# Kernel optimization log

Measured on AMD Instinct MI355X. Metric: run time of the kernel, lower is better.

## Reference

```python
import jax, jax.numpy as jnp
import numpy as np

E, L, M, F, S, P = 4, 10, 512, 128, 1000, 10  # envs, labels, max_sample, features, sample_size, batch_len


def setup_inputs() -> dict:
    key = jax.random.key(0)
    k1, k2, k3 = jax.random.split(key, 3)
    data_len = jax.random.randint(k1, (E, L), M // 2, M + 1, dtype=jnp.int32)
    matrix = jax.random.normal(k2, (E, L, M, F), dtype=jnp.float32)
    # zero out padded samples beyond data_len (as shape_to_matrix does)
    pad_mask = jnp.arange(M)[None, None, :, None] < data_len[:, :, None, None]
    matrix = matrix * pad_mask
    params = jnp.eye(F, dtype=jnp.float32) + 0.01 * jax.random.normal(k3, (F, F), dtype=jnp.float32)
    is_train_env = jnp.array([True, True, False, False])
    return {"matrix": matrix, "params": params, "data_len": data_len, "is_train_env": is_train_env}


def reference(matrix, params, data_len, is_train_env):
    lenf = data_len.astype(matrix.dtype)  # [E,L], torch keeps this as float32
    # __init__ preprocessing: normalize by mean std over sample dim (detached in torch)
    std = jax.lax.stop_gradient(jnp.std(matrix, axis=2).mean())
    mat = matrix / std
    # Silverman-style bandwidth on the normalized matrix (detached in torch)
    bw = jax.lax.stop_gradient(1.06 * (M ** (-1.0 / 5.0)) * jnp.std(mat, axis=2).mean())
    offset = jnp.exp(-0.5 / bw ** 2)
    proj = jnp.einsum('elmf,fg->elmg', mat, params)  # [E,L,M,F]
    left = jax.lax.stop_gradient(proj.min())   # .item() in torch -> constant
    right = jax.lax.stop_gradient(proj.max())
    delta = (right - left) / S
    x_grid = jnp.linspace(left, right, S)
    divisor = jnp.sqrt(2.0 * jnp.pi) * bw

    def step(acc, points):  # points: [P] grid chunk
        d2 = (proj[..., None] - points) ** 2                     # [E,L,M,F,P]
        s = jnp.sum(offset ** d2, axis=2)                        # [E,L,F,P]
        # remove contribution of zero-padded samples, then normalize by true count
        corr = (M - lenf)[:, :, None] * (offset ** (points ** 2))[None, None, :]  # [E,L,P]
        r = (s - corr[:, :, None, :]) / lenf[:, :, None, None]   # [E,L,F,P]
        d = jnp.sum(jnp.abs(r[:, None] - r[None, :]), axis=-1)   # [E,E,L,F] pairwise L1 over grid chunk
        return acc + d, None

    store_dis, _ = jax.lax.scan(step, jnp.zeros((E, E, L, F), proj.dtype), x_grid.reshape(S // P, P))
    store_dis = store_dis / divisor  # [E,E,L,F]

    idx = jnp.arange(E)
    upper = idx[:, None] < idx[None, :]                                   # all env pairs i<j
    train_pair = upper & is_train_env[:, None] & is_train_env[None, :]    # train env pairs i<j
    half = store_dis * (delta / 2.0)
    neg = jnp.array(-jnp.inf, half.dtype)
    test_results = jnp.where(upper[:, :, None, None], half, neg).max(axis=(0, 1))        # [L,F]
    train_results = jnp.where(train_pair[:, :, None, None], half, neg).max(axis=(0, 1))  # [L,F]
    train_dis = train_results.max(axis=0).mean()
    test_dis = test_results.max(axis=0).mean()
    return train_results, test_results, train_dis, test_dis
```

## Files before the change

kernel.cpp:

```cpp
#include <hip/hip_runtime.h>
#include <cmath>

#define E_ 4
#define L_ 10
#define M_ 512
#define F_ 128
#define S_ 1000

typedef unsigned int u32;
typedef _Float16 f16;
typedef __attribute__((ext_vector_type(8))) _Float16 v8h;
typedef __attribute__((ext_vector_type(4))) float v4f;

__device__ __forceinline__ float fexp2(float a){
#if __has_builtin(__builtin_amdgcn_exp2f)
  return __builtin_amdgcn_exp2f(a);
#else
  return exp2f(a);
#endif
}


__global__ __launch_bounds__(256) void k_pre(const float* __restrict__ mat,
                       const float* __restrict__ par,
                       float* __restrict__ projT, float* __restrict__ wsf){
  __shared__ float sm[512];
  int b = blockIdx.x, tid = threadIdx.x;
  if (b >= 1280){
    int el = b - 1280;
    int f = tid & 127, part = tid >> 7;
    const float* base = mat + ((size_t)el * M_ + part*256) * F_;
    float s = 0.f, s2 = 0.f;
    for (int i = 0; i < 256; i++){
      float v = base[i*F_ + f];
      s += v; s2 += v*v;
    }
    sm[tid] = s; sm[256 + tid] = s2;
    __syncthreads();
    if (tid < 128){
      wsf[2576 + el*128 + tid] = sm[tid] + sm[tid+128];
      wsf[7696 + el*128 + tid] = sm[256+tid] + sm[256+tid+128];
    }
    return;
  }
  int el = b >> 5, mt = (b & 31) * 16;
  int lane = tid & 63, wave = tid >> 6;
  int q = (lane >> 4) & 3, m16 = lane & 15;
  const float* arow = mat + ((size_t)el * M_ + mt + m16) * F_;
  v4f acc0 = {0.f,0.f,0.f,0.f}, acc1 = {0.f,0.f,0.f,0.f};
  #pragma unroll
  for (int c = 0; c < 4; c++){
    float4 a0 = *(const float4*)&arow[c*32 + q*8];
    float4 a1 = *(const float4*)&arow[c*32 + q*8 + 4];
    v8h af, b0, b1;
    af[0]=(f16)a0.x; af[1]=(f16)a0.y; af[2]=(f16)a0.z; af[3]=(f16)a0.w;
    af[4]=(f16)a1.x; af[5]=(f16)a1.y; af[6]=(f16)a1.z; af[7]=(f16)a1.w;
    const float* pb = par + (c*32 + q*8)*F_ + wave*32 + m16;
    #pragma unroll
    for (int j = 0; j < 8; j++){
      b0[j] = (f16)pb[j*F_];
      b1[j] = (f16)pb[j*F_ + 16];
    }
    acc0 = __builtin_amdgcn_mfma_f32_16x16x32_f16(af, b0, acc0, 0, 0, 0);
    acc1 = __builtin_amdgcn_mfma_f32_16x16x32_f16(af, b1, acc1, 0, 0, 0);
  }
  *(float4*)(projT + ((size_t)el*F_ + wave*32      + m16)*M_ + mt + q*4)
      = make_float4(acc0[0], acc0[1], acc0[2], acc0[3]);
  *(float4*)(projT + ((size_t)el*F_ + wave*32 + 16 + m16)*M_ + mt + q*4)
      = make_float4(acc1[0], acc1[1], acc1[2], acc1[3]);
  float lmin =  3.4e38f, lmax = -3.4e38f;
  #pragma unroll
  for (int r = 0; r < 4; r++){
    lmin = fminf(lmin, fminf(acc0[r], acc1[r]));
    lmax = fmaxf(lmax, fmaxf(acc0[r], acc1[r]));
  }
  #pragma unroll
  for (int d = 32; d >= 1; d >>= 1){
    lmin = fminf(lmin, __shfl_xor(lmin, d, 64));
    lmax = fmaxf(lmax, __shfl_xor(lmax, d, 64));
  }
  if (lane == 0){ sm[wave] = lmin; sm[8+wave] = lmax; }
  __syncthreads();
  if (tid == 0){
    wsf[16   + b] = fminf(fminf(sm[0], sm[1]), fminf(sm[2], sm[3]));
    wsf[1296 + b] = fmaxf(fmaxf(sm[8], sm[9]), fmaxf(sm[10], sm[11]));
  }
}

__global__ __launch_bounds__(1024) void k_red(float* __restrict__ wsf, float divisor){
  __shared__ float rmn[1024], rmx[1024], rs[1024];
  int tid = threadIdx.x;
  float mn = 3.4e38f, mx = -3.4e38f, s = 0.f;
  for (int i = tid; i < 1280; i += 1024){
    mn = fminf(mn, wsf[16   + i]);
    mx = fmaxf(mx, wsf[1296 + i]);
  }
  for (int i = tid; i < 5120; i += 1024){
    float a  = wsf[2576 + i];
    float a2 = wsf[7696 + i];
    float mean = a * (1.0f/512.0f);
    float var  = a2 * (1.0f/512.0f) - mean*mean;
    s += sqrtf(fmaxf(var, 0.0f));
  }
  rmn[tid] = mn; rmx[tid] = mx; rs[tid] = s;
  __syncthreads();
  for (int g = 512; g >= 1; g >>= 1){
    if (tid < g){
      rmn[tid] = fminf(rmn[tid], rmn[tid+g]);
      rmx[tid] = fmaxf(rmx[tid], rmx[tid+g]);
      rs[tid] += rs[tid+g];
    }
    __syncthreads();
  }
  if (tid == 0){
    float rstd   = 5120.0f / rs[0];
    float leftS  = rmn[0] * rstd;
    float rightS = rmx[0] * rstd;
    float stepFS = (rightS - leftS) * (1.0f/999.0f);
    float inv2   = 1.0f / (2.0f * stepFS);
    wsf[0] = rstd * inv2;
    wsf[1] = leftS * inv2;
    wsf[2] = stepFS;
    wsf[3] = leftS;
    wsf[8] = ((rightS - leftS) * (1.0f/1000.0f)) * 0.5f / divisor;
  }
}

__global__ __launch_bounds__(256) void k_kde(const float* __restrict__ projT,
                      const int* __restrict__ dlen, const float* __restrict__ wsf,
                      float* __restrict__ dpair, float k2c){
  __shared__ __align__(16) float smem[5104];
  int b = blockIdx.x;
  int l = b >> 7, f = b & 127;
  int tid = threadIdx.x, wave = tid >> 6, lane = tid & 63;
  for (int idx = tid; idx < 512; idx += 256){
    int e = idx >> 7, mq = idx & 127;
    ((float4*)smem)[idx] =
      ((const float4*)(projT + (((size_t)e * L_ + l) * F_ + f) * M_))[mq];
  }
  float posScale = wsf[0], posOff = wsf[1], stepFS = wsf[2], leftS = wsf[3];
  for (int idx = tid; idx < 656; idx += 256)
    ((float4*)(smem + 2048))[idx] = make_float4(0.f,0.f,0.f,0.f);
  float sh = 2.0f * stepFS;
  if (tid < 72){
    int u = tid - 34;
    float d0 = (float)(2*u)   * sh;
    float d1 = (float)(2*u-1) * sh;
    float2 t = (tid < 69) ? make_float2(fexp2(k2c*d0*d0), fexp2(k2c*d1*d1))
                          : make_float2(0.f, 0.f);
    *(float2*)&smem[4672 + 2*tid] = t;
  }
  {
    float xc = fmaf((float)(tid - 1), 4.0f*stepFS, leftS);
    smem[4816 + tid] = fexp2(k2c * xc * xc);
  }
  __syncthreads();
  {
    float* hf = smem + 2048 + wave*656;
    const float4* spw4 = (const float4*)(smem + wave*512);
    float4 p0 = spw4[lane], p1 = spw4[lane + 64];
    float pv[8] = {p0.x,p0.y,p0.z,p0.w,p1.x,p1.y,p1.z,p1.w};
    #pragma unroll
    for (int i = 0; i < 8; i++){
      float pos = fmaf(pv[i], posScale, -posOff);
      float n = floorf(pos + 0.5f);
      float d = pos - n;
      float wm = 0.5f*(0.5f-d)*(0.5f-d);
      float wp = 0.5f*(0.5f+d)*(0.5f+d);
      float w0 = 0.75f - d*d;
      int base = (int)n + 71;
      atomicAdd(&hf[base  ], wm);
      atomicAdd(&hf[base+1], w0);
      atomicAdd(&hf[base+2], wp);
    }
  }
  __syncthreads();
  float lenE = (float)dlen[wave*L_ + l];
  float rlen = 1.0f / lenE;
  float padc = 512.0f - lenE;
  {
    const float* sK = smem + 4672;
    const float* hb = smem + 2048 + wave*656;
    float a0=0.f, a1=0.f, a2=0.f, a3=0.f;
    #pragma unroll 8
    for (int uu = 0; uu < 72; uu++){
      float2 kv = *(const float2*)&sK[2*uu];
      int off = 2*(69 - uu) + 2*lane;
      float2 h0 = *(const float2*)&hb[off];
      float2 h1 = *(const float2*)&hb[off + 128];
      float2 h2 = *(const float2*)&hb[off + 256];
      float2 h3 = *(const float2*)&hb[off + 384];
      a0 = fmaf(h0.x, kv.x, fmaf(h0.y, kv.y, a0));
      a1 = fmaf(h1.x, kv.x, fmaf(h1.y, kv.y, a1));
      a2 = fmaf(h2.x, kv.x, fmaf(h2.y, kv.y, a2));
      a3 = fmaf(h3.x, kv.x, fmaf(h3.y, kv.y, a3));
    }
    const float* sCorr = smem + 4816;
    smem[wave*256 + lane      ] = (a0 - padc * sCorr[lane      ]) * rlen;
    smem[wave*256 + lane +  64] = (a1 - padc * sCorr[lane +  64]) * rlen;
    smem[wave*256 + lane + 128] = (a2 - padc * sCorr[lane + 128]) * rlen;
    smem[wave*256 + lane + 192] = (a3 - padc * sCorr[lane + 192]) * rlen;
  }
  __syncthreads();
  float ps[6] = {0,0,0,0,0,0};
  #pragma unroll
  for (int r=0;r<4;r++){
    int t = tid + 256*r;
    if (t < S_){
      int cc = t >> 2;
      float u = (float)(t & 3) * 0.25f;
      float um1 = u - 1.0f, um2 = u - 2.0f, up1 = u + 1.0f;
      float w0 = -u * um1 * um2 * (1.0f/6.0f);
      float w1 = up1 * um1 * um2 * 0.5f;
      float w2 = -u * up1 * um2 * 0.5f;
      float w3 = u * up1 * um1 * (1.0f/6.0f);
      float rr[4];
      #pragma unroll
      for (int e=0;e<4;e++){
        const float* st = &smem[e*256 + cc];
        rr[e] = w0*st[0] + w1*st[1] + w2*st[2] + w3*st[3];
      }
      ps[0] += fabsf(rr[0]-rr[1]);
      ps[1] += fabsf(rr[0]-rr[2]);
      ps[2] += fabsf(rr[0]-rr[3]);
      ps[3] += fabsf(rr[1]-rr[2]);
      ps[4] += fabsf(rr[1]-rr[3]);
      ps[5] += fabsf(rr[2]-rr[3]);
    }
  }
  #pragma unroll
  for (int pr=0; pr<6; pr++){
    float v = ps[pr];
    #pragma unroll
    for (int d=32; d>=1; d>>=1) v += __shfl_xor(v, d, 64);
    if (lane == 0) smem[5072 + wave*8 + pr] = v;
  }
  __syncthreads();
  if (tid < 6)
    dpair[tid*1280 + b] = smem[5072+tid] + smem[5080+tid] + smem[5088+tid] + smem[5096+tid];
}

__global__ void k_fin(const float* __restrict__ dpair, const float* __restrict__ wsf,
                      const int* __restrict__ istrain, float* __restrict__ out){
  __shared__ float str[1280], ste[1280];
  __shared__ float s1[128], s2[128];
  int tid = threadIdx.x;
  float hscale = wsf[8];
  bool t0 = istrain[0]!=0, t1 = istrain[1]!=0, t2 = istrain[2]!=0, t3 = istrain[3]!=0;
  bool trn[6] = { t0&&t1, t0&&t2, t0&&t3, t1&&t2, t1&&t3, t2&&t3 };
  for (int idx = tid; idx < 1280; idx += 256){
    float tmax = -INFINITY, trmax = -INFINITY;
    #pragma unroll
    for (int pr=0;pr<6;pr++){
      float h = dpair[pr*1280 + idx] * hscale;
      tmax = fmaxf(tmax, h);
      if (trn[pr]) trmax = fmaxf(trmax, h);
    }
    out[idx]        = trmax;
    out[1280 + idx] = tmax;
    str[idx] = trmax; ste[idx] = tmax;
  }
  __syncthreads();
  if (tid < 128){
    float m1 = -INFINITY, m2 = -INFINITY;
    for (int l=0;l<L_;l++){
      m1 = fmaxf(m1, str[l*F_ + tid]);
      m2 = fmaxf(m2, ste[l*F_ + tid]);
    }
    s1[tid] = m1; s2[tid] = m2;
  }
  __syncthreads();
  for (int g=64; g>=1; g>>=1){
    if (tid < g){ s1[tid] += s1[tid+g]; s2[tid] += s2[tid+g]; }
    __syncthreads();
  }
  if (tid == 0){
    out[2560] = s1[0] * (1.0f/128.0f);
    out[2561] = s2[0] * (1.0f/128.0f);
  }
}

extern "C" void kernel_launch(void* const* d_in, const int* in_sizes, int n_in,
                              void* d_out, int out_size, void* d_ws, size_t ws_size,
                              hipStream_t stream){
  const float* mat = (const float*)d_in[0];
  const float* par = (const float*)d_in[1];
  const int*  dlen = (const int*)d_in[2];
  const int*  istr = (const int*)d_in[3];
  float* out   = (float*)d_out;
  float* wsf   = (float*)d_ws;
  float* dpair = wsf + 12816;
  float* projT = wsf + 20496;

  double bw_d   = 1.06 * pow(512.0, -0.2);
  float  bw     = (float)bw_d;
  float  offset = expf(-0.5f / (bw*bw));
  float  k2c    = (float)(log((double)offset) * 1.4426950408889634);
  float  divisor = sqrtf(6.283185307179586f) * bw;

  k_pre <<<1320, 256, 0, stream>>>(mat, par, projT, wsf);
  k_red <<<1,   1024, 0, stream>>>(wsf, divisor);
  k_kde <<<1280, 256, 0, stream>>>(projT, dlen, wsf, dpair, k2c);
  k_fin <<<1,    256, 0, stream>>>(dpair, wsf, istr, out);
}
```

Before: 152.7 us.

## Precompute KDE kernel tables once, pad histogram, register-blocked convolution

Moves the exp2-based kernel weights and padding-correction table out of every k_kde block into the single k_red block, so each block copies them from global memory instead of recomputing. The shared histogram gets padding every 8 entries, which is meant to reduce bank conflicts in the atomics and the convolution reads. The convolution now has each lane produce 4 consecutive outputs, with kernel coefficients rotated through registers so each histogram load is reused. The cubic interpolation stage now loads 4 stencil values per thread once and reuses them across 4 sub-positions. The cost is a larger shared allocation, which could lower occupancy, and extra global reads of the tables. It also writes into workspace slots 16..423 that k_pre previously used for block min/max partials; this is safe only because k_red has already consumed them.

```diff
diff --git a/kernel.cpp b/kernel.cpp
--- a/kernel.cpp
+++ b/kernel.cpp
@@ -87,7 +87,8 @@
   }
 }
 
-__global__ __launch_bounds__(1024) void k_red(float* __restrict__ wsf, float divisor){
+__global__ __launch_bounds__(1024) void k_red(float* __restrict__ wsf,
+                                              float divisor, float k2c){
   __shared__ float rmn[1024], rmx[1024], rs[1024];
   int tid = threadIdx.x;
   float mn = 3.4e38f, mx = -3.4e38f, s = 0.f;
@@ -112,52 +113,62 @@
     }
     __syncthreads();
   }
+  float rstd   = 5120.0f / rs[0];
+  float leftS  = rmn[0] * rstd;
+  float rightS = rmx[0] * rstd;
+  float stepFS = (rightS - leftS) * (1.0f/999.0f);
   if (tid == 0){
-    float rstd   = 5120.0f / rs[0];
-    float leftS  = rmn[0] * rstd;
-    float rightS = rmx[0] * rstd;
-    float stepFS = (rightS - leftS) * (1.0f/999.0f);
-    float inv2   = 1.0f / (2.0f * stepFS);
+    float inv2 = 1.0f / (2.0f * stepFS);
     wsf[0] = rstd * inv2;
     wsf[1] = leftS * inv2;
     wsf[2] = stepFS;
     wsf[3] = leftS;
     wsf[8] = ((rightS - leftS) * (1.0f/1000.0f)) * 0.5f / divisor;
   }
+  float sh = 2.0f * stepFS;
+  if (tid < 152){
+    float v = 0.f;
+    if (tid >= 8){
+      int pr = (tid >> 1) - 4;
+      int u  = pr - 34;
+      float d = (tid & 1) ? (float)(2*u-1) * sh : (float)(2*u) * sh;
+      v = (pr < 69) ? fexp2(k2c*d*d) : 0.f;
+    }
+    wsf[16 + tid] = v;
+  }
+  if (tid >= 256 && tid < 512){
+    int idx = tid - 256;
+    float xc = fmaf((float)(idx - 1), 4.0f*stepFS, leftS);
+    wsf[168 + idx] = fexp2(k2c * xc * xc);
+  }
 }
 
 __global__ __launch_bounds__(256) void k_kde(const float* __restrict__ projT,
                       const int* __restrict__ dlen, const float* __restrict__ wsf,
-                      float* __restrict__ dpair, float k2c){
-  __shared__ __align__(16) float smem[5104];
+                      float* __restrict__ dpair){
+  __shared__ __align__(16) float smem[5776];
   int b = blockIdx.x;
   int l = b >> 7, f = b & 127;
   int tid = threadIdx.x, wave = tid >> 6, lane = tid & 63;
-  for (int idx = tid; idx < 512; idx += 256){
-    int e = idx >> 7, mq = idx & 127;
-    ((float4*)smem)[idx] =
-      ((const float4*)(projT + (((size_t)e * L_ + l) * F_ + f) * M_))[mq];
-  }
-  float posScale = wsf[0], posOff = wsf[1], stepFS = wsf[2], leftS = wsf[3];
-  for (int idx = tid; idx < 656; idx += 256)
+  int e = wave;
+  {
+    int e0 = tid >> 7, mq = tid & 127;
+    ((float4*)smem)[tid] =
+      ((const float4*)(projT + (((size_t)e0 * L_ + l) * F_ + f) * M_))[mq];
+    ((float4*)smem)[tid + 256] =
+      ((const float4*)(projT + (((size_t)(e0+2) * L_ + l) * F_ + f) * M_))[mq];
+  }
+  float posScale = wsf[0], posOff = wsf[1];
+  for (int idx = tid; idx < 824; idx += 256)
     ((float4*)(smem + 2048))[idx] = make_float4(0.f,0.f,0.f,0.f);
-  float sh = 2.0f * stepFS;
-  if (tid < 72){
-    int u = tid - 34;
-    float d0 = (float)(2*u)   * sh;
-    float d1 = (float)(2*u-1) * sh;
-    float2 t = (tid < 69) ? make_float2(fexp2(k2c*d0*d0), fexp2(k2c*d1*d1))
-                          : make_float2(0.f, 0.f);
-    *(float2*)&smem[4672 + 2*tid] = t;
-  }
+  if (tid < 38)
+    ((float4*)(smem + 5344))[tid] = ((const float4*)(wsf + 16))[tid];
+  if (tid >= 64 && tid < 128)
+    ((float4*)(smem + 5496))[tid - 64] = ((const float4*)(wsf + 168))[tid - 64];
+  __syncthreads();
   {
-    float xc = fmaf((float)(tid - 1), 4.0f*stepFS, leftS);
-    smem[4816 + tid] = fexp2(k2c * xc * xc);
-  }
-  __syncthreads();
-  {
-    float* hf = smem + 2048 + wave*656;
-    const float4* spw4 = (const float4*)(smem + wave*512);
+    float* hf = smem + 2048 + e*824;
+    const float4* spw4 = (const float4*)(smem + e*512);
     float4 p0 = spw4[lane], p1 = spw4[lane + 64];
     float pv[8] = {p0.x,p0.y,p0.z,p0.w,p1.x,p1.y,p1.z,p1.w};
     #pragma unroll
@@ -168,47 +179,55 @@
       float wm = 0.5f*(0.5f-d)*(0.5f-d);
       float wp = 0.5f*(0.5f+d)*(0.5f+d);
       float w0 = 0.75f - d*d;
-      int base = (int)n + 71;
-      atomicAdd(&hf[base  ], wm);
-      atomicAdd(&hf[base+1], w0);
-      atomicAdd(&hf[base+2], wp);
-    }
-  }
-  __syncthreads();
-  float lenE = (float)dlen[wave*L_ + l];
+      int b0 = (int)n + 71;
+      int b1 = b0 + 1, b2 = b0 + 2;
+      int W0 = b0 + ((b0>>3)<<1);
+      int W1 = b1 + ((b1>>3)<<1);
+      int W2 = b2 + ((b2>>3)<<1);
+      atomicAdd(&hf[W0], wm);
+      atomicAdd(&hf[W1], w0);
+      atomicAdd(&hf[W2], wp);
+    }
+  }
+  __syncthreads();
+  float lenE = (float)dlen[e*L_ + l];
   float rlen = 1.0f / lenE;
   float padc = 512.0f - lenE;
   {
-    const float* sK = smem + 4672;
-    const float* hb = smem + 2048 + wave*656;
+    const float2* sK2 = (const float2*)(smem + 5344);
+    const float* hb = smem + 2048 + e*824;
+    int wb = 8*lane;
+    float2 c0 = sK2[72], c1 = sK2[73], c2 = sK2[74], c3 = sK2[75];
     float a0=0.f, a1=0.f, a2=0.f, a3=0.f;
     #pragma unroll 8
-    for (int uu = 0; uu < 72; uu++){
-      float2 kv = *(const float2*)&sK[2*uu];
-      int off = 2*(69 - uu) + 2*lane;
-      float2 h0 = *(const float2*)&hb[off];
-      float2 h1 = *(const float2*)&hb[off + 128];
-      float2 h2 = *(const float2*)&hb[off + 256];
-      float2 h3 = *(const float2*)&hb[off + 384];
-      a0 = fmaf(h0.x, kv.x, fmaf(h0.y, kv.y, a0));
-      a1 = fmaf(h1.x, kv.x, fmaf(h1.y, kv.y, a1));
-      a2 = fmaf(h2.x, kv.x, fmaf(h2.y, kv.y, a2));
-      a3 = fmaf(h3.x, kv.x, fmaf(h3.y, kv.y, a3));
-    }
-    const float* sCorr = smem + 4816;
-    smem[wave*256 + lane      ] = (a0 - padc * sCorr[lane      ]) * rlen;
-    smem[wave*256 + lane +  64] = (a1 - padc * sCorr[lane +  64]) * rlen;
-    smem[wave*256 + lane + 128] = (a2 - padc * sCorr[lane + 128]) * rlen;
-    smem[wave*256 + lane + 192] = (a3 - padc * sCorr[lane + 192]) * rlen;
+    for (int i = 1; i <= 72; i++){
+      int w  = wb + 2*i;
+      int wp_ = w + ((w>>3)<<1);
+      float2 H = *(const float2*)&hb[wp_];
+      a0 = fmaf(H.x, c0.x, fmaf(H.y, c0.y, a0));
+      a1 = fmaf(H.x, c1.x, fmaf(H.y, c1.y, a1));
+      a2 = fmaf(H.x, c2.x, fmaf(H.y, c2.y, a2));
+      a3 = fmaf(H.x, c3.x, fmaf(H.y, c3.y, a3));
+      c3 = c2; c2 = c1; c1 = c0; c0 = sK2[72 - i];
+    }
+    int o0 = 4*lane;
+    float4 cr = *(const float4*)&smem[5496 + o0];
+    float4 stv = make_float4((a0 - padc*cr.x)*rlen, (a1 - padc*cr.y)*rlen,
+                             (a2 - padc*cr.z)*rlen, (a3 - padc*cr.w)*rlen);
+    *(float4*)&smem[e*256 + o0] = stv;
   }
   __syncthreads();
   float ps[6] = {0,0,0,0,0,0};
-  #pragma unroll
-  for (int r=0;r<4;r++){
-    int t = tid + 256*r;
-    if (t < S_){
-      int cc = t >> 2;
-      float u = (float)(t & 3) * 0.25f;
+  if (tid < 250){
+    float x[4][4];
+    #pragma unroll
+    for (int ee=0; ee<4; ee++){
+      const float* st = &smem[ee*256 + tid];
+      x[ee][0]=st[0]; x[ee][1]=st[1]; x[ee][2]=st[2]; x[ee][3]=st[3];
+    }
+    #pragma unroll
+    for (int k=0; k<4; k++){
+      float u = (float)k * 0.25f;
       float um1 = u - 1.0f, um2 = u - 2.0f, up1 = u + 1.0f;
       float w0 = -u * um1 * um2 * (1.0f/6.0f);
       float w1 = up1 * um1 * um2 * 0.5f;
@@ -216,10 +235,8 @@
       float w3 = u * up1 * um1 * (1.0f/6.0f);
       float rr[4];
       #pragma unroll
-      for (int e=0;e<4;e++){
-        const float* st = &smem[e*256 + cc];
-        rr[e] = w0*st[0] + w1*st[1] + w2*st[2] + w3*st[3];
-      }
+      for (int ee=0; ee<4; ee++)
+        rr[ee] = w0*x[ee][0] + w1*x[ee][1] + w2*x[ee][2] + w3*x[ee][3];
       ps[0] += fabsf(rr[0]-rr[1]);
       ps[1] += fabsf(rr[0]-rr[2]);
       ps[2] += fabsf(rr[0]-rr[3]);
@@ -233,11 +250,11 @@
     float v = ps[pr];
     #pragma unroll
     for (int d=32; d>=1; d>>=1) v += __shfl_xor(v, d, 64);
-    if (lane == 0) smem[5072 + wave*8 + pr] = v;
+    if (lane == 0) smem[5752 + wave*6 + pr] = v;
   }
   __syncthreads();
   if (tid < 6)
-    dpair[tid*1280 + b] = smem[5072+tid] + smem[5080+tid] + smem[5088+tid] + smem[5096+tid];
+    dpair[tid*1280 + b] = smem[5752+tid] + smem[5758+tid] + smem[5764+tid] + smem[5770+tid];
 }
 
 __global__ void k_fin(const float* __restrict__ dpair, const float* __restrict__ wsf,
@@ -299,7 +316,7 @@
   float  divisor = sqrtf(6.283185307179586f) * bw;
 
   k_pre <<<1320, 256, 0, stream>>>(mat, par, projT, wsf);
-  k_red <<<1,   1024, 0, stream>>>(wsf, divisor);
-  k_kde <<<1280, 256, 0, stream>>>(projT, dlen, wsf, dpair, k2c);
+  k_red <<<1,   1024, 0, stream>>>(wsf, divisor, k2c);
+  k_kde <<<1280, 256, 0, stream>>>(projT, dlen, wsf, dpair);
   k_fin <<<1,    256, 0, stream>>>(dpair, wsf, istr, out);
 }
```

After: 143.8 us. 1.06x faster.
